# Performance work log

Hardware: AMD Instinct MI355X
Metric: run time of the kernel (lower is better)

The kernel has to match this reference:

```python
import jax, jax.numpy as jnp
import numpy as np
import math

BATCH, SEQ_LEN, HIDDEN, STATE = 4, 2048, 1024, 64
N2 = STATE // 2  # complex modes
LOG_DT_MIN, LOG_DT_MAX = math.log(0.001), math.log(0.01)


def setup_inputs() -> dict:
    key = jax.random.key(0)
    ks = jax.random.split(key, 6)
    inp = jax.random.normal(ks[0], (BATCH, SEQ_LEN, HIDDEN), dtype=jnp.float32)
    log_dt = jax.random.uniform(ks[1], (HIDDEN,), dtype=jnp.float32) * (LOG_DT_MAX - LOG_DT_MIN) + LOG_DT_MIN
    D = jax.random.normal(ks[2], (HIDDEN,), dtype=jnp.float32)
    # s4d-lin init: A = 0.5 + i*pi*n, param stores log(real) and imag separately
    A_log = jnp.full((HIDDEN, N2), math.log(0.5), dtype=jnp.float32)
    A_imag = jnp.broadcast_to(math.pi * jnp.arange(N2, dtype=jnp.float32), (HIDDEN, N2)).copy()
    B = jax.random.normal(ks[3], (HIDDEN, N2, 2), dtype=jnp.float32)  # view_as_real of cfloat
    C = jax.random.normal(ks[4], (HIDDEN, N2, 2), dtype=jnp.float32)
    return {"input": inp, "log_dt": log_dt, "D": D, "A_log": A_log, "A_imag": A_imag, "B": B, "C": C}


def reference(input, log_dt, D, A_log, A_imag, B, C):
    dt = jnp.exp(log_dt)[:, None]                      # [H,1]
    A = -jnp.exp(A_log) + 1j * A_imag                  # [H,N2] complex, diagonal of diag_embed(A)
    # gbt (bilinear, alpha=0.5) on diagonal A:
    denom = 1.0 - dt / 2.0 * A
    A_disc = (1.0 + dt / 2.0 * A) / denom              # [H,N2]
    Bc = B[..., 0] + 1j * B[..., 1]                    # view_as_complex
    B_disc = dt * Bc / denom                           # [H,N2]
    Cc = (C[..., 0] + 1j * C[..., 1]) * 2.0            # [H,N2]

    x0 = jnp.zeros((input.shape[0], A_disc.shape[0], A_disc.shape[1]), dtype=A_disc.dtype)  # [B,H,N2]
    us = jnp.transpose(input, (1, 0, 2))               # [L,B,H]

    def step(x, u):
        # x_t = A x_{t-1} + B u_t (diagonal A => elementwise)
        x = A_disc * x + B_disc * u[:, :, None]
        y = jnp.einsum('hn,bhn->bh', Cc, x).real + D * u
        return x, y

    _, ys = jax.lax.scan(step, x0, us)                 # ys: [L,B,H]
    return jnp.transpose(ys, (1, 0, 2))                # [B,L,H]
```

## Files before the change

kernel.cpp:

```cpp
#include <hip/hip_runtime.h>
#include <math.h>

#define SEQLEN   2048
#define HIDDEN   1024
#define NMODES   32
#define CHANNELS 4096
#define CHB      16
#define TPG      1024
#define XP       72
#define CSTR     1032

typedef float  f2    __attribute__((ext_vector_type(2)));
typedef short  s8v   __attribute__((ext_vector_type(8)));
typedef float  f32x4 __attribute__((ext_vector_type(4)));
union Frag { s8v s; unsigned u[4]; };

#define SZ_V  (1024*64*64*2)
#define SZ_M  (1024*64*64*2)
#define SZ_K  (1024*64*4)
#define SZ_Q  (1024*64*4)
#define OFF_M (SZ_V)
#define OFF_K (OFF_M + SZ_M)
#define OFF_Q (OFF_K + SZ_K)
#define OFF_C (OFF_Q + SZ_Q)
#define SZ_C  (CHANNELS*64*4)
#define OFF_F (OFF_C + SZ_C)

template <int CTRL>
__device__ __forceinline__ float dpp_add(float p) {
    int t = __builtin_amdgcn_update_dpp(0, __float_as_int(p), CTRL, 0xF, 0xF, true);
    return p + __int_as_float(t);
}
template <int CTRL>
__device__ __forceinline__ float dpp_shr(float x) {
    int t = __builtin_amdgcn_update_dpp(0, __float_as_int(x), CTRL, 0xF, 0xF, true);
    return __int_as_float(t);
}
__device__ __forceinline__ float sum32_to16(float p) {
    p = dpp_add<0xB1>(p); p = dpp_add<0x4E>(p);
    p = dpp_add<0x124>(p); p = dpp_add<0x128>(p);
    p = dpp_add<0x142>(p);
    return p;
}
__device__ __forceinline__ unsigned cvt_pk_bf16(float lo, float hi) {
    unsigned d; asm("v_cvt_pk_bf16_f32 %0, %1, %2" : "=v"(d) : "v"(lo), "v"(hi)); return d;
}
__device__ __forceinline__ unsigned short bf16of(float x) {
    return (unsigned short)(cvt_pk_bf16(x, x) & 0xffffu);
}
__device__ __forceinline__ float bf2f(unsigned s) {
    return __uint_as_float(s << 16);
}

__device__ __forceinline__ void coef1(
    const float* __restrict__ log_dt, const float* __restrict__ A_log,
    const float* __restrict__ A_imag, const float* __restrict__ Bp,
    const float* __restrict__ Cp, int h, int m,
    float& adr, float& adi, float& bpr, float& bpi)
{
    const int idx = h * NMODES + m;
    const float dt = expf(log_dt[h]);
    const float hd = 0.5f * dt;
    const float ar = -expf(A_log[idx]);
    const float ai = A_imag[idx];
    const float dr = 1.f - hd * ar, di = -hd * ai;
    const float inv = 1.f / (dr * dr + di * di);
    const float nr = 1.f + hd * ar, ni = hd * ai;
    adr = (nr * dr + ni * di) * inv;
    adi = (ni * dr - nr * di) * inv;
    const float tbr = dt * Bp[idx * 2], tbi = dt * Bp[idx * 2 + 1];
    const float bdr = (tbr * dr + tbi * di) * inv;
    const float bdi = (tbi * dr - tbr * di) * inv;
    const float cr = 2.f * Cp[idx * 2], ci = 2.f * Cp[idx * 2 + 1];
    bpr = cr * bdr - ci * bdi;
    bpi = cr * bdi + ci * bdr;
}

__global__ __launch_bounds__(256) void ssm_tables(
    const float* __restrict__ log_dt, const float* __restrict__ Dp,
    const float* __restrict__ A_log, const float* __restrict__ A_imag,
    const float* __restrict__ Bp, const float* __restrict__ Cp,
    unsigned short* __restrict__ Vt, unsigned short* __restrict__ Mt,
    float* __restrict__ kct, float* __restrict__ Qt)
{
    const int h = blockIdx.x >> 3, dg = blockIdx.x & 7;
    const int tid = threadIdx.x, wv = tid >> 6, l = tid & 63;
    const int m = l & 31;
    const int d = (dg * 4 + wv) * 2 + (l >> 5);

    float adr, adi, bpr, bpi;
    coef1(log_dt, A_log, A_imag, Bp, Cp, h, m, adr, adi, bpr, bpi);

    float Pr = 1.f, Pi = 0.f, Qr = adr, Qi = adi;
    #pragma unroll
    for (int bit = 0; bit < 6; ++bit) {
        if ((d >> bit) & 1) { float t = Pr*Qr - Pi*Qi; Pi = Pr*Qi + Pi*Qr; Pr = t; }
        float tq = Qr*Qr - Qi*Qi; Qi = 2.f*Qr*Qi; Qr = tq;
    }
    const float wr  = Pr*bpr - Pi*bpi, wi  = Pr*bpi + Pi*bpr;
    const float apr = Pr*adr - Pi*adi, api = Pr*adi + Pi*adr;

    const size_t hb = (size_t)h * 64;
    Vt[(hb + m)      * 64 + (63 - d)] = bf16of(wr);
    Vt[(hb + 32 + m) * 64 + (63 - d)] = bf16of(wi);
    Mt[(hb + d) * 64 + m]       = bf16of(apr);
    Mt[(hb + d) * 64 + 32 + m]  = bf16of(-api);
    if (d == 63) {
        Qt[hb + m]      = apr;
        Qt[hb + 32 + m] = api;
    }

    float s = sum32_to16(wr);
    if ((l & 31) == 16) kct[hb + d] = s + (d == 0 ? Dp[h] : 0.f);
}

__device__ __forceinline__ void stage_frag_u(
    const float* __restrict__ ug, unsigned short* __restrict__ ubuf, int tid)
{
    #pragma unroll
    for (int it = 0; it < 16; ++it) {
        const int t_l = it * 64 + (tid >> 2);
        const int c4  = (tid & 3) * 4;
        const float4 g = *(const float4*)(ug + (size_t)t_l * HIDDEN + c4);
        const int n = t_l >> 6, rr = t_l & 63, ksw = rr >> 5, r5 = rr & 31;
        const int lane = (r5 >> 3) * 16 + n, j = r5 & 7;
        const int base = (ksw * 64 + lane) * 8 + j;
        ubuf[(c4 + 0) * CSTR + base] = bf16of(g.x);
        ubuf[(c4 + 1) * CSTR + base] = bf16of(g.y);
        ubuf[(c4 + 2) * CSTR + base] = bf16of(g.z);
        ubuf[(c4 + 3) * CSTR + base] = bf16of(g.w);
    }
    __syncthreads();
}

__global__ __launch_bounds__(256) void ssm_fused(
    const float* __restrict__ input,
    const unsigned short* __restrict__ Vt, const unsigned short* __restrict__ Mt,
    const float* __restrict__ kct, const float* __restrict__ Qt,
    float* __restrict__ carry, int* __restrict__ flags, float* __restrict__ out)
{
    __shared__ __align__(16) unsigned short ubuf[CHB * CSTR];
    __shared__ float kcP[CHB][128];
    __shared__ __align__(16) unsigned short xbuf[CHB][17][XP];

    const int tid = threadIdx.x, wv = tid >> 6, l = tid & 63;
    const int cgp = blockIdx.x >> 8;
    const int chb = blockIdx.x & 255;
    const int chbase = chb * CHB;
    const int b = chbase >> 10, h0 = chbase & (HIDDEN - 1);
    const int lr = l & 15, lk8 = ((l >> 4) & 3) * 8, lo = (l >> 4) * 4;

    #pragma unroll
    for (int q = 0; q < 8; ++q) {
        const int idx = q * 256 + tid, chl = idx >> 7, k = idx & 127;
        kcP[chl][k] = (k < 64) ? kct[(size_t)(h0 + chl) * 64 + (63 - k)] : 0.f;
    }
    stage_frag_u(input + ((size_t)b * SEQLEN + cgp * TPG) * HIDDEN + h0, ubuf, tid);

    f32x4 acc_s[4][4];
    #pragma unroll
    for (int c = 0; c < 4; ++c) {
        const int chl = wv * 4 + c, h = h0 + chl;
        Frag UB0, UB1;
        UB0.s = *(const s8v*)(ubuf + chl * CSTR + l * 8);
        UB1.s = *(const s8v*)(ubuf + chl * CSTR + (64 + l) * 8);
        #pragma unroll
        for (int mt = 0; mt < 4; ++mt) { f32x4 z = {0.f,0.f,0.f,0.f}; acc_s[c][mt] = z; }
        const unsigned short* Vh = Vt + (size_t)h * 4096;
        #pragma unroll
        for (int mt = 0; mt < 4; ++mt) {
            Frag VA0, VA1;
            VA0.s = *(const s8v*)(Vh + (16 * mt + lr) * 64 + lk8);
            VA1.s = *(const s8v*)(Vh + (16 * mt + lr) * 64 + 32 + lk8);
            acc_s[c][mt] = __builtin_amdgcn_mfma_f32_16x16x32_bf16(VA0.s, UB0.s, acc_s[c][mt], 0, 0, 0);
            acc_s[c][mt] = __builtin_amdgcn_mfma_f32_16x16x32_bf16(VA1.s, UB1.s, acc_s[c][mt], 0, 0, 0);
        }
    }

    if (cgp == 1) {
        if (tid == 0)
            while (__hip_atomic_load(&flags[chb], __ATOMIC_ACQUIRE,
                                     __HIP_MEMORY_SCOPE_AGENT) == 0)
                __builtin_amdgcn_s_sleep(2);
        __syncthreads();
    }

    #pragma unroll
    for (int c = 0; c < 4; ++c) {
        const int chl = wv * 4 + c, ch = chbase + chl, h = h0 + chl;
        float QrA[4], QiA[4], QrB[4], QiB[4];
        {
            const float* qb = Qt + (size_t)h * 64;
            #pragma unroll
            for (int r = 0; r < 4; ++r) {
                QrA[r] = qb[lo + r];      QrB[r] = qb[16 + lo + r];
                QiA[r] = qb[32 + lo + r]; QiB[r] = qb[48 + lo + r];
            }
        }

        float CrA[4] = {0,0,0,0}, CiA[4] = {0,0,0,0}, CrB[4] = {0,0,0,0}, CiB[4] = {0,0,0,0};
        if (cgp == 1 && lr == 0) {
            const float* cb = carry + (size_t)ch * 64;
            #pragma unroll
            for (int r = 0; r < 4; ++r) {
                CrA[r] = cb[lo + r];      CrB[r] = cb[16 + lo + r];
                CiA[r] = cb[32 + lo + r]; CiB[r] = cb[48 + lo + r];
            }
            #pragma unroll
            for (int r = 0; r < 4; ++r) {
                acc_s[c][0][r] += QrA[r]*CrA[r] - QiA[r]*CiA[r];
                acc_s[c][2][r] += QrA[r]*CiA[r] + QiA[r]*CrA[r];
                acc_s[c][1][r] += QrB[r]*CrB[r] - QiB[r]*CiB[r];
                acc_s[c][3][r] += QrB[r]*CiB[r] + QiB[r]*CrB[r];
            }
        }

        #define PSTEP(CTRL) { \
            float Y0[4], Y1[4], Y2[4], Y3[4]; \
            _Pragma("unroll") for (int r = 0; r < 4; ++r) { \
                Y0[r] = dpp_shr<CTRL>(acc_s[c][0][r]); Y1[r] = dpp_shr<CTRL>(acc_s[c][1][r]); \
                Y2[r] = dpp_shr<CTRL>(acc_s[c][2][r]); Y3[r] = dpp_shr<CTRL>(acc_s[c][3][r]); } \
            _Pragma("unroll") for (int r = 0; r < 4; ++r) { \
                acc_s[c][0][r] += QrA[r]*Y0[r] - QiA[r]*Y2[r]; \
                acc_s[c][2][r] += QrA[r]*Y2[r] + QiA[r]*Y0[r]; \
                acc_s[c][1][r] += QrB[r]*Y1[r] - QiB[r]*Y3[r]; \
                acc_s[c][3][r] += QrB[r]*Y3[r] + QiB[r]*Y1[r]; } }
        #define QSQ { _Pragma("unroll") for (int r = 0; r < 4; ++r) { \
            float tA = QrA[r]*QrA[r] - QiA[r]*QiA[r]; QiA[r] = 2.f*QrA[r]*QiA[r]; QrA[r] = tA; \
            float tB = QrB[r]*QrB[r] - QiB[r]*QiB[r]; QiB[r] = 2.f*QrB[r]*QiB[r]; QrB[r] = tB; } }
        PSTEP(0x111) QSQ
        PSTEP(0x112) QSQ
        PSTEP(0x114) QSQ
        PSTEP(0x118)
        #undef PSTEP
        #undef QSQ

        #pragma unroll
        for (int mt = 0; mt < 4; ++mt) {
            *(unsigned*)&xbuf[chl][lr + 1][16*mt + lo]     = cvt_pk_bf16(acc_s[c][mt][0], acc_s[c][mt][1]);
            *(unsigned*)&xbuf[chl][lr + 1][16*mt + lo + 2] = cvt_pk_bf16(acc_s[c][mt][2], acc_s[c][mt][3]);
        }
        if (lr == 0) {
            *(unsigned*)&xbuf[chl][0][lo]          = cvt_pk_bf16(CrA[0], CrA[1]);
            *(unsigned*)&xbuf[chl][0][lo + 2]      = cvt_pk_bf16(CrA[2], CrA[3]);
            *(unsigned*)&xbuf[chl][0][16 + lo]     = cvt_pk_bf16(CrB[0], CrB[1]);
            *(unsigned*)&xbuf[chl][0][16 + lo + 2] = cvt_pk_bf16(CrB[2], CrB[3]);
            *(unsigned*)&xbuf[chl][0][32 + lo]     = cvt_pk_bf16(CiA[0], CiA[1]);
            *(unsigned*)&xbuf[chl][0][32 + lo + 2] = cvt_pk_bf16(CiA[2], CiA[3]);
            *(unsigned*)&xbuf[chl][0][48 + lo]     = cvt_pk_bf16(CiB[0], CiB[1]);
            *(unsigned*)&xbuf[chl][0][48 + lo + 2] = cvt_pk_bf16(CiB[2], CiB[3]);
        }
        if (cgp == 0 && lr == 15) {
            float* cb = carry + (size_t)ch * 64;
            #pragma unroll
            for (int r = 0; r < 4; ++r) {
                cb[lo + r]      = acc_s[c][0][r];
                cb[16 + lo + r] = acc_s[c][1][r];
                cb[32 + lo + r] = acc_s[c][2][r];
                cb[48 + lo + r] = acc_s[c][3][r];
            }
        }
    }

    if (cgp == 0) {
        __syncthreads();
        if (tid == 0) {
            __threadfence();
            __hip_atomic_store(&flags[chb], 1, __ATOMIC_RELEASE,
                               __HIP_MEMORY_SCOPE_AGENT);
        }
    }
    __syncthreads();

    f32x4 acc[4][4];
    #pragma unroll
    for (int c = 0; c < 4; ++c) {
        const int chl = wv * 4 + c, h = h0 + chl;
        Frag UB[2];
        UB[0].s = *(const s8v*)(ubuf + chl * CSTR + l * 8);
        UB[1].s = *(const s8v*)(ubuf + chl * CSTR + (64 + l) * 8);

        #pragma unroll
        for (int mt = 0; mt < 4; ++mt) { f32x4 z = {0.f,0.f,0.f,0.f}; acc[c][mt] = z; }

        Frag XB[2];
        XB[0].s = *(const s8v*)&xbuf[chl][lr][lk8];
        XB[1].s = *(const s8v*)&xbuf[chl][lr][32 + lk8];

        #pragma unroll
        for (int ks = 0; ks < 2; ++ks) {
            #pragma unroll
            for (int mt = 0; mt < 4; ++mt) {
                const int base = 63 - 16 * mt + 32 * ks + lk8 - lr;
                float f[8];
                #pragma unroll
                for (int j = 0; j < 8; ++j) f[j] = kcP[chl][base + j];
                Frag TA;
                #pragma unroll
                for (int q = 0; q < 4; ++q) TA.u[q] = cvt_pk_bf16(f[2*q], f[2*q+1]);
                acc[c][mt] = __builtin_amdgcn_mfma_f32_16x16x32_bf16(
                    TA.s, UB[ks].s, acc[c][mt], 0, 0, 0);
            }
        }
        const unsigned short* Mh = Mt + (size_t)h * 4096;
        #pragma unroll
        for (int ks = 0; ks < 2; ++ks) {
            #pragma unroll
            for (int mt = 0; mt < 4; ++mt) {
                Frag MA; MA.s = *(const s8v*)(Mh + (16 * mt + lr) * 64 + ks * 32 + lk8);
                acc[c][mt] = __builtin_amdgcn_mfma_f32_16x16x32_bf16(
                    MA.s, XB[ks].s, acc[c][mt], 0, 0, 0);
            }
        }
    }

    float* ob = out + ((size_t)b * SEQLEN + cgp * TPG) * HIDDEN + h0;
    #pragma unroll
    for (int half = 0; half < 2; ++half) {
        __syncthreads();
        if ((lr >> 3) == half) {
            const int lr7 = lr & 7;
            #pragma unroll
            for (int c = 0; c < 4; ++c) {
                const int chl = wv * 4 + c;
                const int col = chl ^ (lr7 << 1);
                #pragma unroll
                for (int mt = 0; mt < 4; ++mt)
                    #pragma unroll
                    for (int r = 0; r < 4; ++r) {
                        const int t_loc = lr7 * 64 + 16 * mt + lo + r;
                        ubuf[t_loc * 32 + col] = bf16of(acc[c][mt][r]);
                    }
            }
        }
        __syncthreads();
        float* obh = ob + (size_t)half * 512 * HIDDEN;
        #pragma unroll
        for (int q = 0; q < 8; ++q) {
            const int idx = q * 256 + tid;
            const int t_loc = idx >> 2, a = idx & 3;
            const int lrt = (t_loc >> 6) & 7;
            const int blk = (a ^ (lrt >> 1)) * 4;
            const uint2 w = *(const uint2*)(ubuf + t_loc * 32 + blk);
            const float s0 = bf2f(w.x & 0xffffu), s1 = bf2f(w.x >> 16);
            const float s2 = bf2f(w.y & 0xffffu), s3 = bf2f(w.y >> 16);
            float4 o;
            if (lrt & 1) o = make_float4(s2, s3, s0, s1);
            else         o = make_float4(s0, s1, s2, s3);
            *(float4*)(obh + (size_t)t_loc * HIDDEN + a * 4) = o;
        }
    }
}

extern "C" void kernel_launch(void* const* d_in, const int* in_sizes, int n_in,
                              void* d_out, int out_size, void* d_ws, size_t ws_size,
                              hipStream_t stream) {
    const float* input  = (const float*)d_in[0];
    const float* log_dt = (const float*)d_in[1];
    const float* Dp     = (const float*)d_in[2];
    const float* A_log  = (const float*)d_in[3];
    const float* A_imag = (const float*)d_in[4];
    const float* Bp     = (const float*)d_in[5];
    const float* Cp     = (const float*)d_in[6];
    float* out = (float*)d_out;

    unsigned short* Vt  = (unsigned short*)d_ws;
    unsigned short* Mtb = (unsigned short*)((char*)d_ws + OFF_M);
    float*          kct = (float*)((char*)d_ws + OFF_K);
    float*          Qt  = (float*)((char*)d_ws + OFF_Q);
    float*          carry = (float*)((char*)d_ws + OFF_C);
    int*            flags = (int*)((char*)d_ws + OFF_F);

    hipMemsetAsync(flags, 0, 256 * sizeof(int), stream);
    ssm_tables<<<dim3(1024 * 8), dim3(256), 0, stream>>>(
        log_dt, Dp, A_log, A_imag, Bp, Cp, Vt, Mtb, kct, Qt);
    ssm_fused<<<dim3(512), dim3(256), 0, stream>>>(
        input, Vt, Mtb, kct, Qt, carry, flags, out);
}
```

Before: 81.07 us.

## Defer carry wait past the local scan and Toeplitz MFMA to hide latency

```diff
diff --git a/kernel.cpp b/kernel.cpp
--- a/kernel.cpp
+++ b/kernel.cpp
@@ -177,14 +177,6 @@
         }
     }
 
-    if (cgp == 1) {
-        if (tid == 0)
-            while (__hip_atomic_load(&flags[chb], __ATOMIC_ACQUIRE,
-                                     __HIP_MEMORY_SCOPE_AGENT) == 0)
-                __builtin_amdgcn_s_sleep(2);
-        __syncthreads();
-    }
-
     #pragma unroll
     for (int c = 0; c < 4; ++c) {
         const int chl = wv * 4 + c, ch = chbase + chl, h = h0 + chl;
@@ -195,23 +187,6 @@
             for (int r = 0; r < 4; ++r) {
                 QrA[r] = qb[lo + r];      QrB[r] = qb[16 + lo + r];
                 QiA[r] = qb[32 + lo + r]; QiB[r] = qb[48 + lo + r];
-            }
-        }
-
-        float CrA[4] = {0,0,0,0}, CiA[4] = {0,0,0,0}, CrB[4] = {0,0,0,0}, CiB[4] = {0,0,0,0};
-        if (cgp == 1 && lr == 0) {
-            const float* cb = carry + (size_t)ch * 64;
-            #pragma unroll
-            for (int r = 0; r < 4; ++r) {
-                CrA[r] = cb[lo + r];      CrB[r] = cb[16 + lo + r];
-                CiA[r] = cb[32 + lo + r]; CiB[r] = cb[48 + lo + r];
-            }
-            #pragma unroll
-            for (int r = 0; r < 4; ++r) {
-                acc_s[c][0][r] += QrA[r]*CrA[r] - QiA[r]*CiA[r];
-                acc_s[c][2][r] += QrA[r]*CiA[r] + QiA[r]*CrA[r];
-                acc_s[c][1][r] += QrB[r]*CrB[r] - QiB[r]*CiB[r];
-                acc_s[c][3][r] += QrB[r]*CiB[r] + QiB[r]*CrB[r];
             }
         }
 
@@ -235,29 +210,28 @@
         #undef PSTEP
         #undef QSQ
 
-        #pragma unroll
-        for (int mt = 0; mt < 4; ++mt) {
-            *(unsigned*)&xbuf[chl][lr + 1][16*mt + lo]     = cvt_pk_bf16(acc_s[c][mt][0], acc_s[c][mt][1]);
-            *(unsigned*)&xbuf[chl][lr + 1][16*mt + lo + 2] = cvt_pk_bf16(acc_s[c][mt][2], acc_s[c][mt][3]);
-        }
-        if (lr == 0) {
-            *(unsigned*)&xbuf[chl][0][lo]          = cvt_pk_bf16(CrA[0], CrA[1]);
-            *(unsigned*)&xbuf[chl][0][lo + 2]      = cvt_pk_bf16(CrA[2], CrA[3]);
-            *(unsigned*)&xbuf[chl][0][16 + lo]     = cvt_pk_bf16(CrB[0], CrB[1]);
-            *(unsigned*)&xbuf[chl][0][16 + lo + 2] = cvt_pk_bf16(CrB[2], CrB[3]);
-            *(unsigned*)&xbuf[chl][0][32 + lo]     = cvt_pk_bf16(CiA[0], CiA[1]);
-            *(unsigned*)&xbuf[chl][0][32 + lo + 2] = cvt_pk_bf16(CiA[2], CiA[3]);
-            *(unsigned*)&xbuf[chl][0][48 + lo]     = cvt_pk_bf16(CiB[0], CiB[1]);
-            *(unsigned*)&xbuf[chl][0][48 + lo + 2] = cvt_pk_bf16(CiB[2], CiB[3]);
-        }
-        if (cgp == 0 && lr == 15) {
-            float* cb = carry + (size_t)ch * 64;
-            #pragma unroll
-            for (int r = 0; r < 4; ++r) {
-                cb[lo + r]      = acc_s[c][0][r];
-                cb[16 + lo + r] = acc_s[c][1][r];
-                cb[32 + lo + r] = acc_s[c][2][r];
-                cb[48 + lo + r] = acc_s[c][3][r];
+        if (cgp == 0) {
+            #pragma unroll
+            for (int mt = 0; mt < 4; ++mt) {
+                *(unsigned*)&xbuf[chl][lr + 1][16*mt + lo]     = cvt_pk_bf16(acc_s[c][mt][0], acc_s[c][mt][1]);
+                *(unsigned*)&xbuf[chl][lr + 1][16*mt + lo + 2] = cvt_pk_bf16(acc_s[c][mt][2], acc_s[c][mt][3]);
+            }
+            if (lr == 0) {
+                #pragma unroll
+                for (int g2 = 0; g2 < 4; ++g2) {
+                    *(unsigned*)&xbuf[chl][0][16*g2 + lo]     = 0u;
+                    *(unsigned*)&xbuf[chl][0][16*g2 + lo + 2] = 0u;
+                }
+            }
+            if (lr == 15) {
+                float* cb = carry + (size_t)ch * 64;
+                #pragma unroll
+                for (int r = 0; r < 4; ++r) {
+                    cb[lo + r]      = acc_s[c][0][r];
+                    cb[16 + lo + r] = acc_s[c][1][r];
+                    cb[32 + lo + r] = acc_s[c][2][r];
+                    cb[48 + lo + r] = acc_s[c][3][r];
+                }
             }
         }
     }
@@ -270,38 +244,112 @@
                                __HIP_MEMORY_SCOPE_AGENT);
         }
     }
+
+    f32x4 acc[4][4];
+    Frag UBk[4][2];
+    #pragma unroll
+    for (int c = 0; c < 4; ++c) {
+        const int chl = wv * 4 + c;
+        UBk[c][0].s = *(const s8v*)(ubuf + chl * CSTR + l * 8);
+        UBk[c][1].s = *(const s8v*)(ubuf + chl * CSTR + (64 + l) * 8);
+        #pragma unroll
+        for (int mt = 0; mt < 4; ++mt) { f32x4 z = {0.f,0.f,0.f,0.f}; acc[c][mt] = z; }
+        #pragma unroll
+        for (int ks = 0; ks < 2; ++ks) {
+            #pragma unroll
+            for (int mt = 0; mt < 4; ++mt) {
+                const int base = 63 - 16 * mt + 32 * ks + lk8 - lr;
+                float f[8];
+                #pragma unroll
+                for (int j = 0; j < 8; ++j) f[j] = kcP[chl][base + j];
+                Frag TA;
+                #pragma unroll
+                for (int q = 0; q < 4; ++q) TA.u[q] = cvt_pk_bf16(f[2*q], f[2*q+1]);
+                acc[c][mt] = __builtin_amdgcn_mfma_f32_16x16x32_bf16(
+                    TA.s, UBk[c][ks].s, acc[c][mt], 0, 0, 0);
+            }
+        }
+    }
+
+    if (cgp == 1) {
+        if (tid == 0)
+            while (__hip_atomic_load(&flags[chb], __ATOMIC_ACQUIRE,
+                                     __HIP_MEMORY_SCOPE_AGENT) == 0)
+                __builtin_amdgcn_s_sleep(2);
+        __syncthreads();
+
+        #pragma unroll
+        for (int c = 0; c < 4; ++c) {
+            const int chl = wv * 4 + c, ch = chbase + chl, h = h0 + chl;
+            float PrA[4], PiA[4], PrB[4], PiB[4];
+            {
+                const float* qb = Qt + (size_t)h * 64;
+                float QrA[4], QiA[4], QrB[4], QiB[4];
+                #pragma unroll
+                for (int r = 0; r < 4; ++r) {
+                    QrA[r] = qb[lo + r];      QrB[r] = qb[16 + lo + r];
+                    QiA[r] = qb[32 + lo + r]; QiB[r] = qb[48 + lo + r];
+                    PrA[r] = 1.f; PiA[r] = 0.f; PrB[r] = 1.f; PiB[r] = 0.f;
+                }
+                const int e = lr + 1;
+                #pragma unroll
+                for (int bit = 0; bit < 5; ++bit) {
+                    const bool on = (e >> bit) & 1;
+                    #pragma unroll
+                    for (int r = 0; r < 4; ++r) {
+                        const float nAr = PrA[r]*QrA[r] - PiA[r]*QiA[r];
+                        const float nAi = PrA[r]*QiA[r] + PiA[r]*QrA[r];
+                        const float nBr = PrB[r]*QrB[r] - PiB[r]*QiB[r];
+                        const float nBi = PrB[r]*QiB[r] + PiB[r]*QrB[r];
+                        PrA[r] = on ? nAr : PrA[r]; PiA[r] = on ? nAi : PiA[r];
+                        PrB[r] = on ? nBr : PrB[r]; PiB[r] = on ? nBi : PiB[r];
+                        const float sAr = QrA[r]*QrA[r] - QiA[r]*QiA[r];
+                        QiA[r] = 2.f*QrA[r]*QiA[r]; QrA[r] = sAr;
+                        const float sBr = QrB[r]*QrB[r] - QiB[r]*QiB[r];
+                        QiB[r] = 2.f*QrB[r]*QiB[r]; QrB[r] = sBr;
+                    }
+                }
+            }
+            const float* cb = carry + (size_t)ch * 64;
+            float CrA[4], CiA[4], CrB[4], CiB[4];
+            #pragma unroll
+            for (int r = 0; r < 4; ++r) {
+                CrA[r] = cb[lo + r];      CrB[r] = cb[16 + lo + r];
+                CiA[r] = cb[32 + lo + r]; CiB[r] = cb[48 + lo + r];
+            }
+            #pragma unroll
+            for (int r = 0; r < 4; ++r) {
+                acc_s[c][0][r] += PrA[r]*CrA[r] - PiA[r]*CiA[r];
+                acc_s[c][2][r] += PrA[r]*CiA[r] + PiA[r]*CrA[r];
+                acc_s[c][1][r] += PrB[r]*CrB[r] - PiB[r]*CiB[r];
+                acc_s[c][3][r] += PrB[r]*CiB[r] + PiB[r]*CrB[r];
+            }
+            #pragma unroll
+            for (int mt = 0; mt < 4; ++mt) {
+                *(unsigned*)&xbuf[chl][lr + 1][16*mt + lo]     = cvt_pk_bf16(acc_s[c][mt][0], acc_s[c][mt][1]);
+                *(unsigned*)&xbuf[chl][lr + 1][16*mt + lo + 2] = cvt_pk_bf16(acc_s[c][mt][2], acc_s[c][mt][3]);
+            }
+            if (lr == 0) {
+                *(unsigned*)&xbuf[chl][0][lo]          = cvt_pk_bf16(CrA[0], CrA[1]);
+                *(unsigned*)&xbuf[chl][0][lo + 2]      = cvt_pk_bf16(CrA[2], CrA[3]);
+                *(unsigned*)&xbuf[chl][0][16 + lo]     = cvt_pk_bf16(CrB[0], CrB[1]);
+                *(unsigned*)&xbuf[chl][0][16 + lo + 2] = cvt_pk_bf16(CrB[2], CrB[3]);
+                *(unsigned*)&xbuf[chl][0][32 + lo]     = cvt_pk_bf16(CiA[0], CiA[1]);
+                *(unsigned*)&xbuf[chl][0][32 + lo + 2] = cvt_pk_bf16(CiA[2], CiA[3]);
+                *(unsigned*)&xbuf[chl][0][48 + lo]     = cvt_pk_bf16(CiB[0], CiB[1]);
+                *(unsigned*)&xbuf[chl][0][48 + lo + 2] = cvt_pk_bf16(CiB[2], CiB[3]);
+            }
+        }
+    }
+
     __syncthreads();
 
-    f32x4 acc[4][4];
     #pragma unroll
     for (int c = 0; c < 4; ++c) {
         const int chl = wv * 4 + c, h = h0 + chl;
-        Frag UB[2];
-        UB[0].s = *(const s8v*)(ubuf + chl * CSTR + l * 8);
-        UB[1].s = *(const s8v*)(ubuf + chl * CSTR + (64 + l) * 8);
-
-        #pragma unroll
-        for (int mt = 0; mt < 4; ++mt) { f32x4 z = {0.f,0.f,0.f,0.f}; acc[c][mt] = z; }
-
         Frag XB[2];
         XB[0].s = *(const s8v*)&xbuf[chl][lr][lk8];
         XB[1].s = *(const s8v*)&xbuf[chl][lr][32 + lk8];
-
-        #pragma unroll
-        for (int ks = 0; ks < 2; ++ks) {
-            #pragma unroll
-            for (int mt = 0; mt < 4; ++mt) {
-                const int base = 63 - 16 * mt + 32 * ks + lk8 - lr;
-                float f[8];
-                #pragma unroll
-                for (int j = 0; j < 8; ++j) f[j] = kcP[chl][base + j];
-                Frag TA;
-                #pragma unroll
-                for (int q = 0; q < 4; ++q) TA.u[q] = cvt_pk_bf16(f[2*q], f[2*q+1]);
-                acc[c][mt] = __builtin_amdgcn_mfma_f32_16x16x32_bf16(
-                    TA.s, UB[ks].s, acc[c][mt], 0, 0, 0);
-            }
-        }
         const unsigned short* Mh = Mt + (size_t)h * 4096;
         #pragma unroll
         for (int ks = 0; ks < 2; ++ks) {
```

Result: slower. 82.98 us (+2.4%).
